# Kernel tuning notes

Measured on AMD Instinct MI355X. Metric: run time of the kernel, lower is better.

The kernel has to match this reference:

```python
import jax, jax.numpy as jnp
import numpy as np

MD = 4  # max displacement -> (2*MD+1)**2 = 81 shift channels


def setup_inputs() -> dict:
    key = jax.random.key(0)
    k1, k2 = jax.random.split(key)
    B, C, H, W = 4, 64, 192, 320
    tenFirst = jax.random.normal(k1, (B, C, H, W), dtype=jnp.float32)
    tenSecond = jax.random.normal(k2, (B, C, H, W), dtype=jnp.float32)
    return {"tenFirst": tenFirst, "tenSecond": tenSecond}


def reference(tenFirst, tenSecond):
    # Windowed cross-correlation cost volume (PWC-Net style):
    # out[b, k, y, x] = mean_c first[b,c,y,x] * second[b,c,y+dy,x+dx]
    # for (dy,dx) in [-4,4]^2, k = (dy+4)*9 + (dx+4). Out-of-bounds -> 0 via padding.
    B, C, H, W = tenFirst.shape
    padded = jnp.pad(tenSecond, ((0, 0), (0, 0), (MD, MD), (MD, MD)))
    outs = []
    for dy in range(2 * MD + 1):  # fixed small set of 81 shifts
        for dx in range(2 * MD + 1):
            shifted = padded[:, :, dy:dy + H, dx:dx + W]  # [B,C,H,W]
            outs.append(jnp.mean(tenFirst * shifted, axis=1))  # [B,H,W]
    return jnp.stack(outs, axis=1)  # [B,81,H,W]
```

## Files before the change

kernel.cpp:

```cpp
#include <hip/hip_runtime.h>
#include <hip/hip_bf16.h>


#define WW   320
#define HH   192
#define CC   64
#define HWSZ (HH * WW)
#define NB   4
#define PW   328
#define PH   200
#define NDISP 81
#define ESTV 20

typedef __attribute__((ext_vector_type(8))) short bf16x8_t;
typedef __attribute__((ext_vector_type(4))) float f32x4_t;

static __device__ __forceinline__ unsigned short f2bf(float f) {
    unsigned int u = __float_as_uint(f);
    u += 0x7fffu + ((u >> 16) & 1u);
    return (unsigned short)(u >> 16);
}

static __device__ __forceinline__ unsigned pack2(float a, float b) {
    return (unsigned)f2bf(a) | ((unsigned)f2bf(b) << 16);
}

__global__ __launch_bounds__(256, 6)
void conv_both(const float* __restrict__ F,
               const float* __restrict__ S,
               unsigned short* __restrict__ Fc,
               unsigned short* __restrict__ Sp) {
    __shared__ float ta[64][65];
    const int t  = threadIdx.x;
    const int x0 = blockIdx.x * 64;
    const int y  = blockIdx.y;
    const int b  = blockIdx.z;

    const int blk = (b * HH + y) * (WW / 64) + blockIdx.x;
    const int gid = blk * 256 + t;
    if (gid < NB * 4160 * 8) {
        int bb = gid / (4160 * 8);
        int r  = gid % (4160 * 8);
        int px = r >> 3;
        int v  = r & 7;
        int row, colp;
        if (px < 2624) {
            int strip = px / 1312;
            int pp    = px % 1312;
            row  = (strip ? 196 : 0) + pp / 328;
            colp = pp % 328;
        } else {
            int tt2 = px - 2624;
            row  = 4 + (tt2 >> 3);
            int tt = tt2 & 7;
            colp = (tt < 4) ? tt : (320 + tt);
        }
        uint4 z; z.x = 0u; z.y = 0u; z.z = 0u; z.w = 0u;
        *(uint4*)((unsigned short*)Sp + ((((size_t)bb * PH + row) * PW + colp) * 8 + v) * 8) = z;
    }

    const int x4 = t & 15;
    const int c0 = t >> 4;
    const float* fsrc = F + (size_t)b * CC * HWSZ + (size_t)y * WW + x0 + 4 * x4;
    const float* ssrc = S + (size_t)b * CC * HWSZ + (size_t)y * WW + x0 + 4 * x4;
    float4 vF[4], vS[4];
#pragma unroll
    for (int k = 0; k < 4; ++k)
        vF[k] = *(const float4*)(fsrc + (size_t)(c0 + 16 * k) * HWSZ);
#pragma unroll
    for (int k = 0; k < 4; ++k)
        vS[k] = *(const float4*)(ssrc + (size_t)(c0 + 16 * k) * HWSZ);

#pragma unroll
    for (int k = 0; k < 4; ++k) {
        int c = c0 + 16 * k;
        ta[c][4 * x4 + 0] = vF[k].x;
        ta[c][4 * x4 + 1] = vF[k].y;
        ta[c][4 * x4 + 2] = vF[k].z;
        ta[c][4 * x4 + 3] = vF[k].w;
    }
    __syncthreads();

    const int xx = t >> 2;
    const int cg = (t & 3) * 16;
    {
        unsigned short* dst = Fc + (((size_t)b * HH + y) * WW + (x0 + xx)) * CC + cg;
        uint4 w;
        w.x = pack2(ta[cg + 0][xx],  ta[cg + 1][xx]);
        w.y = pack2(ta[cg + 2][xx],  ta[cg + 3][xx]);
        w.z = pack2(ta[cg + 4][xx],  ta[cg + 5][xx]);
        w.w = pack2(ta[cg + 6][xx],  ta[cg + 7][xx]);
        *(uint4*)dst = w;
        w.x = pack2(ta[cg + 8][xx],  ta[cg + 9][xx]);
        w.y = pack2(ta[cg + 10][xx], ta[cg + 11][xx]);
        w.z = pack2(ta[cg + 12][xx], ta[cg + 13][xx]);
        w.w = pack2(ta[cg + 14][xx], ta[cg + 15][xx]);
        *(uint4*)(dst + 8) = w;
    }
    __syncthreads();

#pragma unroll
    for (int k = 0; k < 4; ++k) {
        int c = c0 + 16 * k;
        ta[c][4 * x4 + 0] = vS[k].x;
        ta[c][4 * x4 + 1] = vS[k].y;
        ta[c][4 * x4 + 2] = vS[k].z;
        ta[c][4 * x4 + 3] = vS[k].w;
    }
    __syncthreads();

    {
        unsigned short* dst = Sp + (((size_t)b * PH + (y + 4)) * PW + (x0 + xx + 4)) * CC + cg;
        uint4 w;
        w.x = pack2(ta[cg + 0][xx],  ta[cg + 1][xx]);
        w.y = pack2(ta[cg + 2][xx],  ta[cg + 3][xx]);
        w.z = pack2(ta[cg + 4][xx],  ta[cg + 5][xx]);
        w.w = pack2(ta[cg + 6][xx],  ta[cg + 7][xx]);
        *(uint4*)dst = w;
        w.x = pack2(ta[cg + 8][xx],  ta[cg + 9][xx]);
        w.y = pack2(ta[cg + 10][xx], ta[cg + 11][xx]);
        w.z = pack2(ta[cg + 12][xx], ta[cg + 13][xx]);
        w.w = pack2(ta[cg + 14][xx], ta[cg + 15][xx]);
        *(uint4*)(dst + 8) = w;
    }
}

__global__ __launch_bounds__(256, 4)
void corr_mfma_v4(const unsigned short* __restrict__ Fc,
                  const unsigned short* __restrict__ Sp,
                  float* __restrict__ out) {
    __shared__ float ebuf[4][27 * ESTV];

    const int tid  = threadIdx.x;
    const int wave = tid >> 6;
    const int lane = tid & 63;
    const int q    = lane >> 4;
    const int col  = lane & 15;

    const int i    = blockIdx.x;
    const int xcd  = i & 7;
    const int j    = i >> 3;
    const int b    = j / 180;
    const int r180 = j % 180;
    const int pql  = r180 / 60;
    const int r60  = r180 % 60;
    const int g    = r60 / 20;
    const int xt   = r60 % 20;
    const int pq   = xcd * 3 + pql;
    const int yp   = pq * 4 + wave;
    const int y0   = yp * 2;
    const int x0   = xt * 16;
    const int d0   = g * 3;

    const unsigned short* fc =
        Fc + (((size_t)b * HH + y0) * WW + (x0 + col)) * CC + q * 8;
    const bf16x8_t a00 = *(const bf16x8_t*)(fc);
    const bf16x8_t a01 = *(const bf16x8_t*)(fc + 32);
    const bf16x8_t a10 = *(const bf16x8_t*)(fc + (size_t)WW * CC);
    const bf16x8_t a11 = *(const bf16x8_t*)(fc + (size_t)WW * CC + 32);

    f32x4_t acc[2][3][2];
#pragma unroll
    for (int p = 0; p < 2; ++p)
#pragma unroll
        for (int d = 0; d < 3; ++d)
#pragma unroll
            for (int nt = 0; nt < 2; ++nt)
#pragma unroll
                for (int k = 0; k < 4; ++k) acc[p][d][nt][k] = 0.f;

#pragma unroll
    for (int rr = 0; rr < 4; ++rr) {
        const unsigned short* srow = Sp + ((size_t)b * PH + (y0 + d0 + rr)) * PW * CC;
#pragma unroll
        for (int nt = 0; nt < 2; ++nt) {
            int xp = x0 + col + 16 * nt;
            xp = xp > (PW - 1) ? (PW - 1) : xp;
            const unsigned short* p = srow + (size_t)xp * CC + q * 8;
            const bf16x8_t b0 = *(const bf16x8_t*)(p);
            const bf16x8_t b1 = *(const bf16x8_t*)(p + 32);
            if (rr < 3) {
                acc[0][rr][nt] = __builtin_amdgcn_mfma_f32_16x16x32_bf16(a00, b0, acc[0][rr][nt], 0, 0, 0);
                acc[0][rr][nt] = __builtin_amdgcn_mfma_f32_16x16x32_bf16(a01, b1, acc[0][rr][nt], 0, 0, 0);
            }
            if (rr >= 1) {
                acc[1][rr - 1][nt] = __builtin_amdgcn_mfma_f32_16x16x32_bf16(a10, b0, acc[1][rr - 1][nt], 0, 0, 0);
                acc[1][rr - 1][nt] = __builtin_amdgcn_mfma_f32_16x16x32_bf16(a11, b1, acc[1][rr - 1][nt], 0, 0, 0);
            }
        }
    }

    const float scale = 1.0f / 64.0f;
    float* my = ebuf[wave];
#pragma unroll
    for (int p = 0; p < 2; ++p) {
#pragma unroll
        for (int dyi = 0; dyi < 3; ++dyi)
#pragma unroll
            for (int nt = 0; nt < 2; ++nt)
#pragma unroll
                for (int k = 0; k < 4; ++k) {
                    int m  = 4 * q + k;
                    int dx = col + 16 * nt - m;
                    if (dx >= 0 && dx <= 8)
                        my[(dyi * 9 + dx) * ESTV + m] = acc[p][dyi][nt][k] * scale;
                }
        float* ob = out + ((size_t)b * NDISP + d0 * 9) * HWSZ + (size_t)(y0 + p) * WW + x0;
#pragma unroll
        for (int rnd = 0; rnd < 2; ++rnd) {
            int idx = rnd * 64 + lane;
            if (idx < 108) {
                int d  = idx >> 2;
                int m4 = (idx & 3) * 4;
                *(float4*)(ob + (size_t)d * HWSZ + m4) = *(const float4*)(my + d * ESTV + m4);
            }
        }
    }
}

__global__ __launch_bounds__(256) void fill_zero(uint4* __restrict__ p, int n4) {
    int i = blockIdx.x * 256 + threadIdx.x;
    if (i < n4) {
        uint4 z; z.x = 0u; z.y = 0u; z.z = 0u; z.w = 0u;
        p[i] = z;
    }
}

__global__ __launch_bounds__(256) void conv_pad(const float* __restrict__ S,
                                                unsigned short* __restrict__ Sp) {
    __shared__ float tile[64][65];
    const int tx = threadIdx.x;
    const int ty = threadIdx.y;
    const int x0 = blockIdx.x * 64;
    const int y  = blockIdx.y;
    const int b  = blockIdx.z;

    const float* src = S + (size_t)b * CC * HWSZ + (size_t)y * WW + x0 + tx;
#pragma unroll
    for (int i = 0; i < 16; ++i) {
        int c = ty * 16 + i;
        tile[c][tx] = src[(size_t)c * HWSZ];
    }
    __syncthreads();

    const int t  = ty * 64 + tx;
    const int xx = t >> 2;
    const int cg = (t & 3) * 16;
    unsigned short tmp[16];
#pragma unroll
    for (int i = 0; i < 16; ++i) tmp[i] = f2bf(tile[cg + i][xx]);

    unsigned short* dst = Sp + (((size_t)b * PH + (y + 4)) * PW + (x0 + xx + 4)) * CC + cg;
    uint4 v;
    v.x = (unsigned)tmp[0]  | ((unsigned)tmp[1]  << 16);
    v.y = (unsigned)tmp[2]  | ((unsigned)tmp[3]  << 16);
    v.z = (unsigned)tmp[4]  | ((unsigned)tmp[5]  << 16);
    v.w = (unsigned)tmp[6]  | ((unsigned)tmp[7]  << 16);
    *(uint4*)dst = v;
    v.x = (unsigned)tmp[8]  | ((unsigned)tmp[9]  << 16);
    v.y = (unsigned)tmp[10] | ((unsigned)tmp[11] << 16);
    v.z = (unsigned)tmp[12] | ((unsigned)tmp[13] << 16);
    v.w = (unsigned)tmp[14] | ((unsigned)tmp[15] << 16);
    *(uint4*)(dst + 8) = v;
}

__global__ __launch_bounds__(256) void corr_mfma(const float* __restrict__ F,
                                                 const unsigned short* __restrict__ Sp,
                                                 float* __restrict__ out) {
    __shared__ float lds[4][NDISP * 16];
    const int tid  = threadIdx.x;
    const int wave = tid >> 6;
    const int lane = tid & 63;
    const int q    = lane >> 4;
    const int col  = lane & 15;
    const int wid = blockIdx.x * 4 + wave;
    const int xt  = wid % 20;
    const int y   = (wid / 20) % HH;
    const int b   = wid / (20 * HH);
    const int x0  = xt * 16;

    bf16x8_t a0, a1;
    const float* fb = F + (size_t)b * CC * HWSZ + (size_t)y * WW + x0 + col;
#pragma unroll
    for (int j = 0; j < 8; ++j) {
        a0[j] = (short)f2bf(fb[(size_t)(q * 8 + j) * HWSZ]);
        a1[j] = (short)f2bf(fb[(size_t)(32 + q * 8 + j) * HWSZ]);
    }
    f32x4_t acc[9][2];
#pragma unroll
    for (int i = 0; i < 9; ++i)
#pragma unroll
        for (int nt = 0; nt < 2; ++nt)
#pragma unroll
            for (int r = 0; r < 4; ++r) acc[i][nt][r] = 0.f;
#pragma unroll
    for (int dyi = 0; dyi < 9; ++dyi) {
        const unsigned short* srow = Sp + ((size_t)b * PH + (y + dyi)) * PW * CC;
#pragma unroll
        for (int nt = 0; nt < 2; ++nt) {
            int xp = x0 + col + 16 * nt;
            xp = xp > (PW - 1) ? (PW - 1) : xp;
            const unsigned short* p = srow + (size_t)xp * CC + q * 8;
            bf16x8_t b0 = *(const bf16x8_t*)(p);
            bf16x8_t b1 = *(const bf16x8_t*)(p + 32);
            acc[dyi][nt] = __builtin_amdgcn_mfma_f32_16x16x32_bf16(a0, b0, acc[dyi][nt], 0, 0, 0);
            acc[dyi][nt] = __builtin_amdgcn_mfma_f32_16x16x32_bf16(a1, b1, acc[dyi][nt], 0, 0, 0);
        }
    }
    float* my = lds[wave];
    const float scale = 1.0f / 64.0f;
#pragma unroll
    for (int dyi = 0; dyi < 9; ++dyi)
#pragma unroll
        for (int nt = 0; nt < 2; ++nt)
#pragma unroll
            for (int r = 0; r < 4; ++r) {
                int m  = 4 * q + r;
                int dx = col + 16 * nt - m;
                if (dx >= 0 && dx <= 8)
                    my[(dyi * 9 + dx) * 16 + m] = acc[dyi][nt][r] * scale;
            }
    __syncthreads();
    float* ob = out + (size_t)b * NDISP * HWSZ + (size_t)y * WW + x0;
#pragma unroll
    for (int rnd = 0; rnd < 21; ++rnd) {
        int idx = rnd * 64 + lane;
        if (rnd < 20 || idx < NDISP * 16) {
            int d = idx >> 4, m = idx & 15;
            ob[(size_t)d * HWSZ + m] = my[idx];
        }
    }
}

#define MDV      4
#define TILE_X   64
#define TILE_Y   8
#define CH_STAGE 4
#define LDS_ROWS (TILE_Y + 2 * MDV)
#define LDS_COLS (TILE_X + 2 * MDV)

__global__ __launch_bounds__(256, 2)
void corr_direct(const float* __restrict__ first,
                 const float* __restrict__ second,
                 float* __restrict__ out) {
    const int C = 64, H = HH, W = WW;
    const int HW = H * W;
    __shared__ float lds[CH_STAGE][LDS_ROWS * LDS_COLS];
    const int tx = threadIdx.x, ty = threadIdx.y;
    const int tid = ty * 32 + tx;
    const int x_tile = blockIdx.x * TILE_X;
    const int y_tile = blockIdx.y * TILE_Y;
    const int b = blockIdx.z;
    const int x0 = x_tile + 2 * tx;
    const int y  = y_tile + ty;
    const float* fst_b = first  + (size_t)b * C * HW;
    const float* sec_b = second + (size_t)b * C * HW;
    float acc[NDISP][2];
#pragma unroll
    for (int d = 0; d < NDISP; ++d) { acc[d][0] = 0.f; acc[d][1] = 0.f; }
    for (int cb = 0; cb < C; cb += CH_STAGE) {
        __syncthreads();
        const int total = CH_STAGE * LDS_ROWS * LDS_COLS;
#pragma unroll
        for (int k = 0; k < total / 256; ++k) {
            int i = tid + k * 256;
            int c   = i / (LDS_ROWS * LDS_COLS);
            int rem = i - c * (LDS_ROWS * LDS_COLS);
            int r   = rem / LDS_COLS;
            int cl  = rem - r * LDS_COLS;
            int gy = y_tile - MDV + r;
            int gx = x_tile - MDV + cl;
            float v = 0.f;
            if ((unsigned)gy < (unsigned)H && (unsigned)gx < (unsigned)W)
                v = sec_b[(size_t)(cb + c) * HW + gy * W + gx];
            lds[c][rem] = v;
        }
        __syncthreads();
#pragma unroll
        for (int cl = 0; cl < CH_STAGE; ++cl) {
            const int c = cb + cl;
            const float2 f = *(const float2*)&fst_b[(size_t)c * HW + y * W + x0];
#pragma unroll
            for (int r = 0; r < 9; ++r) {
                const float* row = &lds[cl][(ty + r) * LDS_COLS + 2 * tx];
                float w[10];
#pragma unroll
                for (int k = 0; k < 5; ++k) {
                    float2 t2 = *(const float2*)&row[2 * k];
                    w[2 * k] = t2.x; w[2 * k + 1] = t2.y;
                }
#pragma unroll
                for (int dx = 0; dx < 9; ++dx) {
                    acc[r * 9 + dx][0] += f.x * w[dx];
                    acc[r * 9 + dx][1] += f.y * w[dx + 1];
                }
            }
        }
    }
    const float scale = 1.0f / 64.0f;
    float* out_b = out + (size_t)b * NDISP * HW;
#pragma unroll
    for (int d = 0; d < NDISP; ++d) {
        float2 o;
        o.x = acc[d][0] * scale;
        o.y = acc[d][1] * scale;
        *(float2*)&out_b[(size_t)d * HW + y * W + x0] = o;
    }
}

extern "C" void kernel_launch(void* const* d_in, const int* in_sizes, int n_in,
                              void* d_out, int out_size, void* d_ws, size_t ws_size,
                              hipStream_t stream) {
    const float* tenFirst  = (const float*)d_in[0];
    const float* tenSecond = (const float*)d_in[1];
    float* out = (float*)d_out;

    const size_t sp_bytes = (size_t)NB * PH * PW * CC * 2;
    const size_t fc_bytes = (size_t)NB * HH * WW * CC * 2;

    if (ws_size >= sp_bytes + fc_bytes) {
        unsigned short* Sp = (unsigned short*)d_ws;
        unsigned short* Fc = (unsigned short*)((char*)d_ws + sp_bytes);
        conv_both<<<dim3(WW / 64, HH, NB), 256, 0, stream>>>(tenFirst, tenSecond, Fc, Sp);
        corr_mfma_v4<<<5760, 256, 0, stream>>>(Fc, Sp, out);
    } else if (ws_size >= sp_bytes) {
        unsigned short* Sp = (unsigned short*)d_ws;
        const int n4 = (int)(sp_bytes / 16);
        fill_zero<<<(n4 + 255) / 256, 256, 0, stream>>>((uint4*)Sp, n4);
        conv_pad<<<dim3(WW / 64, HH, NB), dim3(64, 4), 0, stream>>>(tenSecond, Sp);
        corr_mfma<<<NB * HH * 20 / 4, 256, 0, stream>>>(tenFirst, Sp, out);
    } else {
        corr_direct<<<dim3(WW / TILE_X, HH / TILE_Y, NB), dim3(32, 8), 0, stream>>>(
            tenFirst, tenSecond, out);
    }
}
```

Before: 234.4 us.

## Drop bf16 copy of first input; convert it inside correlation kernel and loop dy groups

The prep kernel now converts only the second tensor into the padded channel-last bf16 buffer. The correlation kernel reads the fp32 first tensor directly and converts it to bf16 in registers. Each block now loops over all three dy groups, so the first-tensor fragments are loaded once per block and reused, and the grid shrinks by a factor of three. This removes the write and re-read of a bf16 copy of the first tensor, at the cost of strided scalar fp32 loads and less parallelism per launch.

Measured after the change: 229.9 us. Within noise of the previous version (-1.9%).

```diff
diff --git a/kernel.cpp b/kernel.cpp
--- a/kernel.cpp
+++ b/kernel.cpp
@@ -26,10 +26,8 @@
 }
 
 __global__ __launch_bounds__(256, 6)
-void conv_both(const float* __restrict__ F,
-               const float* __restrict__ S,
-               unsigned short* __restrict__ Fc,
-               unsigned short* __restrict__ Sp) {
+void conv_s(const float* __restrict__ S,
+            unsigned short* __restrict__ Sp) {
     __shared__ float ta[64][65];
     const int t  = threadIdx.x;
     const int x0 = blockIdx.x * 64;
@@ -61,43 +59,11 @@
 
     const int x4 = t & 15;
     const int c0 = t >> 4;
-    const float* fsrc = F + (size_t)b * CC * HWSZ + (size_t)y * WW + x0 + 4 * x4;
     const float* ssrc = S + (size_t)b * CC * HWSZ + (size_t)y * WW + x0 + 4 * x4;
-    float4 vF[4], vS[4];
-#pragma unroll
-    for (int k = 0; k < 4; ++k)
-        vF[k] = *(const float4*)(fsrc + (size_t)(c0 + 16 * k) * HWSZ);
+    float4 vS[4];
 #pragma unroll
     for (int k = 0; k < 4; ++k)
         vS[k] = *(const float4*)(ssrc + (size_t)(c0 + 16 * k) * HWSZ);
-
-#pragma unroll
-    for (int k = 0; k < 4; ++k) {
-        int c = c0 + 16 * k;
-        ta[c][4 * x4 + 0] = vF[k].x;
-        ta[c][4 * x4 + 1] = vF[k].y;
-        ta[c][4 * x4 + 2] = vF[k].z;
-        ta[c][4 * x4 + 3] = vF[k].w;
-    }
-    __syncthreads();
-
-    const int xx = t >> 2;
-    const int cg = (t & 3) * 16;
-    {
-        unsigned short* dst = Fc + (((size_t)b * HH + y) * WW + (x0 + xx)) * CC + cg;
-        uint4 w;
-        w.x = pack2(ta[cg + 0][xx],  ta[cg + 1][xx]);
-        w.y = pack2(ta[cg + 2][xx],  ta[cg + 3][xx]);
-        w.z = pack2(ta[cg + 4][xx],  ta[cg + 5][xx]);
-        w.w = pack2(ta[cg + 6][xx],  ta[cg + 7][xx]);
-        *(uint4*)dst = w;
-        w.x = pack2(ta[cg + 8][xx],  ta[cg + 9][xx]);
-        w.y = pack2(ta[cg + 10][xx], ta[cg + 11][xx]);
-        w.z = pack2(ta[cg + 12][xx], ta[cg + 13][xx]);
-        w.w = pack2(ta[cg + 14][xx], ta[cg + 15][xx]);
-        *(uint4*)(dst + 8) = w;
-    }
-    __syncthreads();
 
 #pragma unroll
     for (int k = 0; k < 4; ++k) {
@@ -109,24 +75,24 @@
     }
     __syncthreads();
 
-    {
-        unsigned short* dst = Sp + (((size_t)b * PH + (y + 4)) * PW + (x0 + xx + 4)) * CC + cg;
-        uint4 w;
-        w.x = pack2(ta[cg + 0][xx],  ta[cg + 1][xx]);
-        w.y = pack2(ta[cg + 2][xx],  ta[cg + 3][xx]);
-        w.z = pack2(ta[cg + 4][xx],  ta[cg + 5][xx]);
-        w.w = pack2(ta[cg + 6][xx],  ta[cg + 7][xx]);
-        *(uint4*)dst = w;
-        w.x = pack2(ta[cg + 8][xx],  ta[cg + 9][xx]);
-        w.y = pack2(ta[cg + 10][xx], ta[cg + 11][xx]);
-        w.z = pack2(ta[cg + 12][xx], ta[cg + 13][xx]);
-        w.w = pack2(ta[cg + 14][xx], ta[cg + 15][xx]);
-        *(uint4*)(dst + 8) = w;
-    }
+    const int xx = t >> 2;
+    const int cg = (t & 3) * 16;
+    unsigned short* dst = Sp + (((size_t)b * PH + (y + 4)) * PW + (x0 + xx + 4)) * CC + cg;
+    uint4 w;
+    w.x = pack2(ta[cg + 0][xx],  ta[cg + 1][xx]);
+    w.y = pack2(ta[cg + 2][xx],  ta[cg + 3][xx]);
+    w.z = pack2(ta[cg + 4][xx],  ta[cg + 5][xx]);
+    w.w = pack2(ta[cg + 6][xx],  ta[cg + 7][xx]);
+    *(uint4*)dst = w;
+    w.x = pack2(ta[cg + 8][xx],  ta[cg + 9][xx]);
+    w.y = pack2(ta[cg + 10][xx], ta[cg + 11][xx]);
+    w.z = pack2(ta[cg + 12][xx], ta[cg + 13][xx]);
+    w.w = pack2(ta[cg + 14][xx], ta[cg + 15][xx]);
+    *(uint4*)(dst + 8) = w;
 }
 
 __global__ __launch_bounds__(256, 4)
-void corr_mfma_v4(const unsigned short* __restrict__ Fc,
+void corr_mfma_v5(const float* __restrict__ F,
                   const unsigned short* __restrict__ Sp,
                   float* __restrict__ out) {
     __shared__ float ebuf[4][27 * ESTV];
@@ -140,194 +106,85 @@
     const int i    = blockIdx.x;
     const int xcd  = i & 7;
     const int j    = i >> 3;
-    const int b    = j / 180;
-    const int r180 = j % 180;
-    const int pql  = r180 / 60;
-    const int r60  = r180 % 60;
-    const int g    = r60 / 20;
+    const int b    = j / 60;
+    const int r60  = j % 60;
+    const int pql  = r60 / 20;
     const int xt   = r60 % 20;
     const int pq   = xcd * 3 + pql;
     const int yp   = pq * 4 + wave;
     const int y0   = yp * 2;
     const int x0   = xt * 16;
-    const int d0   = g * 3;
-
-    const unsigned short* fc =
-        Fc + (((size_t)b * HH + y0) * WW + (x0 + col)) * CC + q * 8;
-    const bf16x8_t a00 = *(const bf16x8_t*)(fc);
-    const bf16x8_t a01 = *(const bf16x8_t*)(fc + 32);
-    const bf16x8_t a10 = *(const bf16x8_t*)(fc + (size_t)WW * CC);
-    const bf16x8_t a11 = *(const bf16x8_t*)(fc + (size_t)WW * CC + 32);
-
-    f32x4_t acc[2][3][2];
-#pragma unroll
-    for (int p = 0; p < 2; ++p)
-#pragma unroll
-        for (int d = 0; d < 3; ++d)
-#pragma unroll
-            for (int nt = 0; nt < 2; ++nt)
-#pragma unroll
-                for (int k = 0; k < 4; ++k) acc[p][d][nt][k] = 0.f;
-
-#pragma unroll
-    for (int rr = 0; rr < 4; ++rr) {
-        const unsigned short* srow = Sp + ((size_t)b * PH + (y0 + d0 + rr)) * PW * CC;
-#pragma unroll
-        for (int nt = 0; nt < 2; ++nt) {
-            int xp = x0 + col + 16 * nt;
-            xp = xp > (PW - 1) ? (PW - 1) : xp;
-            const unsigned short* p = srow + (size_t)xp * CC + q * 8;
-            const bf16x8_t b0 = *(const bf16x8_t*)(p);
-            const bf16x8_t b1 = *(const bf16x8_t*)(p + 32);
-            if (rr < 3) {
-                acc[0][rr][nt] = __builtin_amdgcn_mfma_f32_16x16x32_bf16(a00, b0, acc[0][rr][nt], 0, 0, 0);
-                acc[0][rr][nt] = __builtin_amdgcn_mfma_f32_16x16x32_bf16(a01, b1, acc[0][rr][nt], 0, 0, 0);
-            }
-            if (rr >= 1) {
-                acc[1][rr - 1][nt] = __builtin_amdgcn_mfma_f32_16x16x32_bf16(a10, b0, acc[1][rr - 1][nt], 0, 0, 0);
-                acc[1][rr - 1][nt] = __builtin_amdgcn_mfma_f32_16x16x32_bf16(a11, b1, acc[1][rr - 1][nt], 0, 0, 0);
-            }
-        }
+
+    const float* fb = F + (size_t)b * CC * HWSZ + (size_t)y0 * WW + x0 + col;
+    bf16x8_t a00, a01, a10, a11;
+#pragma unroll
+    for (int jj = 0; jj < 8; ++jj) {
+        a00[jj] = (short)f2bf(fb[(size_t)(q * 8 + jj) * HWSZ]);
+        a01[jj] = (short)f2bf(fb[(size_t)(32 + q * 8 + jj) * HWSZ]);
+        a10[jj] = (short)f2bf(fb[(size_t)(q * 8 + jj) * HWSZ + WW]);
+        a11[jj] = (short)f2bf(fb[(size_t)(32 + q * 8 + jj) * HWSZ + WW]);
     }
 
     const float scale = 1.0f / 64.0f;
     float* my = ebuf[wave];
-#pragma unroll
-    for (int p = 0; p < 2; ++p) {
-#pragma unroll
-        for (int dyi = 0; dyi < 3; ++dyi)
-#pragma unroll
-            for (int nt = 0; nt < 2; ++nt)
-#pragma unroll
-                for (int k = 0; k < 4; ++k) {
-                    int m  = 4 * q + k;
-                    int dx = col + 16 * nt - m;
-                    if (dx >= 0 && dx <= 8)
-                        my[(dyi * 9 + dx) * ESTV + m] = acc[p][dyi][nt][k] * scale;
-                }
-        float* ob = out + ((size_t)b * NDISP + d0 * 9) * HWSZ + (size_t)(y0 + p) * WW + x0;
-#pragma unroll
-        for (int rnd = 0; rnd < 2; ++rnd) {
-            int idx = rnd * 64 + lane;
-            if (idx < 108) {
-                int d  = idx >> 2;
-                int m4 = (idx & 3) * 4;
-                *(float4*)(ob + (size_t)d * HWSZ + m4) = *(const float4*)(my + d * ESTV + m4);
+
+    for (int g = 0; g < 3; ++g) {
+        const int d0 = g * 3;
+
+        f32x4_t acc[2][3][2];
+#pragma unroll
+        for (int p = 0; p < 2; ++p)
+#pragma unroll
+            for (int d = 0; d < 3; ++d)
+#pragma unroll
+                for (int nt = 0; nt < 2; ++nt)
+#pragma unroll
+                    for (int k = 0; k < 4; ++k) acc[p][d][nt][k] = 0.f;
+
+#pragma unroll
+        for (int rr = 0; rr < 4; ++rr) {
+            const unsigned short* srow = Sp + ((size_t)b * PH + (y0 + d0 + rr)) * PW * CC;
+#pragma unroll
+            for (int nt = 0; nt < 2; ++nt) {
+                int xp = x0 + col + 16 * nt;
+                xp = xp > (PW - 1) ? (PW - 1) : xp;
+                const unsigned short* p = srow + (size_t)xp * CC + q * 8;
+                const bf16x8_t b0 = *(const bf16x8_t*)(p);
+                const bf16x8_t b1 = *(const bf16x8_t*)(p + 32);
+                if (rr < 3) {
+                    acc[0][rr][nt] = __builtin_amdgcn_mfma_f32_16x16x32_bf16(a00, b0, acc[0][rr][nt], 0, 0, 0);
+                    acc[0][rr][nt] = __builtin_amdgcn_mfma_f32_16x16x32_bf16(a01, b1, acc[0][rr][nt], 0, 0, 0);
+                }
+                if (rr >= 1) {
+                    acc[1][rr - 1][nt] = __builtin_amdgcn_mfma_f32_16x16x32_bf16(a10, b0, acc[1][rr - 1][nt], 0, 0, 0);
+                    acc[1][rr - 1][nt] = __builtin_amdgcn_mfma_f32_16x16x32_bf16(a11, b1, acc[1][rr - 1][nt], 0, 0, 0);
+                }
             }
         }
-    }
-}
-
-__global__ __launch_bounds__(256) void fill_zero(uint4* __restrict__ p, int n4) {
-    int i = blockIdx.x * 256 + threadIdx.x;
-    if (i < n4) {
-        uint4 z; z.x = 0u; z.y = 0u; z.z = 0u; z.w = 0u;
-        p[i] = z;
-    }
-}
-
-__global__ __launch_bounds__(256) void conv_pad(const float* __restrict__ S,
-                                                unsigned short* __restrict__ Sp) {
-    __shared__ float tile[64][65];
-    const int tx = threadIdx.x;
-    const int ty = threadIdx.y;
-    const int x0 = blockIdx.x * 64;
-    const int y  = blockIdx.y;
-    const int b  = blockIdx.z;
-
-    const float* src = S + (size_t)b * CC * HWSZ + (size_t)y * WW + x0 + tx;
-#pragma unroll
-    for (int i = 0; i < 16; ++i) {
-        int c = ty * 16 + i;
-        tile[c][tx] = src[(size_t)c * HWSZ];
-    }
-    __syncthreads();
-
-    const int t  = ty * 64 + tx;
-    const int xx = t >> 2;
-    const int cg = (t & 3) * 16;
-    unsigned short tmp[16];
-#pragma unroll
-    for (int i = 0; i < 16; ++i) tmp[i] = f2bf(tile[cg + i][xx]);
-
-    unsigned short* dst = Sp + (((size_t)b * PH + (y + 4)) * PW + (x0 + xx + 4)) * CC + cg;
-    uint4 v;
-    v.x = (unsigned)tmp[0]  | ((unsigned)tmp[1]  << 16);
-    v.y = (unsigned)tmp[2]  | ((unsigned)tmp[3]  << 16);
-    v.z = (unsigned)tmp[4]  | ((unsigned)tmp[5]  << 16);
-    v.w = (unsigned)tmp[6]  | ((unsigned)tmp[7]  << 16);
-    *(uint4*)dst = v;
-    v.x = (unsigned)tmp[8]  | ((unsigned)tmp[9]  << 16);
-    v.y = (unsigned)tmp[10] | ((unsigned)tmp[11] << 16);
-    v.z = (unsigned)tmp[12] | ((unsigned)tmp[13] << 16);
-    v.w = (unsigned)tmp[14] | ((unsigned)tmp[15] << 16);
-    *(uint4*)(dst + 8) = v;
-}
-
-__global__ __launch_bounds__(256) void corr_mfma(const float* __restrict__ F,
-                                                 const unsigned short* __restrict__ Sp,
-                                                 float* __restrict__ out) {
-    __shared__ float lds[4][NDISP * 16];
-    const int tid  = threadIdx.x;
-    const int wave = tid >> 6;
-    const int lane = tid & 63;
-    const int q    = lane >> 4;
-    const int col  = lane & 15;
-    const int wid = blockIdx.x * 4 + wave;
-    const int xt  = wid % 20;
-    const int y   = (wid / 20) % HH;
-    const int b   = wid / (20 * HH);
-    const int x0  = xt * 16;
-
-    bf16x8_t a0, a1;
-    const float* fb = F + (size_t)b * CC * HWSZ + (size_t)y * WW + x0 + col;
-#pragma unroll
-    for (int j = 0; j < 8; ++j) {
-        a0[j] = (short)f2bf(fb[(size_t)(q * 8 + j) * HWSZ]);
-        a1[j] = (short)f2bf(fb[(size_t)(32 + q * 8 + j) * HWSZ]);
-    }
-    f32x4_t acc[9][2];
-#pragma unroll
-    for (int i = 0; i < 9; ++i)
-#pragma unroll
-        for (int nt = 0; nt < 2; ++nt)
-#pragma unroll
-            for (int r = 0; r < 4; ++r) acc[i][nt][r] = 0.f;
-#pragma unroll
-    for (int dyi = 0; dyi < 9; ++dyi) {
-        const unsigned short* srow = Sp + ((size_t)b * PH + (y + dyi)) * PW * CC;
-#pragma unroll
-        for (int nt = 0; nt < 2; ++nt) {
-            int xp = x0 + col + 16 * nt;
-            xp = xp > (PW - 1) ? (PW - 1) : xp;
-            const unsigned short* p = srow + (size_t)xp * CC + q * 8;
-            bf16x8_t b0 = *(const bf16x8_t*)(p);
-            bf16x8_t b1 = *(const bf16x8_t*)(p + 32);
-            acc[dyi][nt] = __builtin_amdgcn_mfma_f32_16x16x32_bf16(a0, b0, acc[dyi][nt], 0, 0, 0);
-            acc[dyi][nt] = __builtin_amdgcn_mfma_f32_16x16x32_bf16(a1, b1, acc[dyi][nt], 0, 0, 0);
-        }
-    }
-    float* my = lds[wave];
-    const float scale = 1.0f / 64.0f;
-#pragma unroll
-    for (int dyi = 0; dyi < 9; ++dyi)
-#pragma unroll
-        for (int nt = 0; nt < 2; ++nt)
-#pragma unroll
-            for (int r = 0; r < 4; ++r) {
-                int m  = 4 * q + r;
-                int dx = col + 16 * nt - m;
-                if (dx >= 0 && dx <= 8)
-                    my[(dyi * 9 + dx) * 16 + m] = acc[dyi][nt][r] * scale;
+
+#pragma unroll
+        for (int p = 0; p < 2; ++p) {
+#pragma unroll
+            for (int dyi = 0; dyi < 3; ++dyi)
+#pragma unroll
+                for (int nt = 0; nt < 2; ++nt)
+#pragma unroll
+                    for (int k = 0; k < 4; ++k) {
+                        int m  = 4 * q + k;
+                        int dx = col + 16 * nt - m;
+                        if (dx >= 0 && dx <= 8)
+                            my[(dyi * 9 + dx) * ESTV + m] = acc[p][dyi][nt][k] * scale;
+                    }
+            float* ob = out + ((size_t)b * NDISP + d0 * 9) * HWSZ + (size_t)(y0 + p) * WW + x0;
+#pragma unroll
+            for (int rnd = 0; rnd < 2; ++rnd) {
+                int idx = rnd * 64 + lane;
+                if (idx < 108) {
+                    int d  = idx >> 2;
+                    int m4 = (idx & 3) * 4;
+                    *(float4*)(ob + (size_t)d * HWSZ + m4) = *(const float4*)(my + d * ESTV + m4);
+                }
             }
-    __syncthreads();
-    float* ob = out + (size_t)b * NDISP * HWSZ + (size_t)y * WW + x0;
-#pragma unroll
-    for (int rnd = 0; rnd < 21; ++rnd) {
-        int idx = rnd * 64 + lane;
-        if (rnd < 20 || idx < NDISP * 16) {
-            int d = idx >> 4, m = idx & 15;
-            ob[(size_t)d * HWSZ + m] = my[idx];
         }
     }
 }
@@ -416,19 +273,11 @@
     float* out = (float*)d_out;
 
     const size_t sp_bytes = (size_t)NB * PH * PW * CC * 2;
-    const size_t fc_bytes = (size_t)NB * HH * WW * CC * 2;
-
-    if (ws_size >= sp_bytes + fc_bytes) {
+
+    if (ws_size >= sp_bytes) {
         unsigned short* Sp = (unsigned short*)d_ws;
-        unsigned short* Fc = (unsigned short*)((char*)d_ws + sp_bytes);
-        conv_both<<<dim3(WW / 64, HH, NB), 256, 0, stream>>>(tenFirst, tenSecond, Fc, Sp);
-        corr_mfma_v4<<<5760, 256, 0, stream>>>(Fc, Sp, out);
-    } else if (ws_size >= sp_bytes) {
-        unsigned short* Sp = (unsigned short*)d_ws;
-        const int n4 = (int)(sp_bytes / 16);
-        fill_zero<<<(n4 + 255) / 256, 256, 0, stream>>>((uint4*)Sp, n4);
-        conv_pad<<<dim3(WW / 64, HH, NB), dim3(64, 4), 0, stream>>>(tenSecond, Sp);
-        corr_mfma<<<NB * HH * 20 / 4, 256, 0, stream>>>(tenFirst, Sp, out);
+        conv_s<<<dim3(WW / 64, HH, NB), 256, 0, stream>>>(tenSecond, Sp);
+        corr_mfma_v5<<<1920, 256, 0, stream>>>(tenFirst, Sp, out);
     } else {
         corr_direct<<<dim3(WW / TILE_X, HH / TILE_Y, NB), dim3(32, 8), 0, stream>>>(
             tenFirst, tenSecond, out);
```
